# Kernel tuning notes

Hardware: AMD Instinct MI355X
Metric: run time of the kernel (lower is better)

The kernel has to match this reference:

```python
import jax, jax.numpy as jnp
import numpy as np

T, D, E = 16384, 4096, 64  # tokens, hidden dim, num experts


def setup_inputs() -> dict:
    key = jax.random.key(0)
    kx, kw = jax.random.split(key)
    x = jax.random.normal(kx, (T, D), dtype=jnp.float32)
    W = jax.random.normal(kw, (E, D), dtype=jnp.float32) * (1.0 / np.sqrt(D))
    b = jnp.zeros((E,), dtype=jnp.float32)
    return {"x": x, "W": W, "b": b}


def reference(x, W, b):
    # Linear: [T, D] @ [D, E] + [E] -> [T, E]
    logits = jnp.einsum("td,ed->te", x, W) + b
    probs = jax.nn.softmax(logits, axis=-1)
    # Top-2 selection over experts
    top2_vals, top2_idx = jax.lax.top_k(probs, 2)  # [T, 2]
    # Note: original applies softmax (not sum-renorm) to the top-2 probs
    norm2 = jax.nn.softmax(top2_vals, axis=-1)  # [T, 2]
    # Scatter back into a dense [T, E] gating distribution
    gating = jnp.zeros_like(probs)
    rows = jnp.arange(T)[:, None]
    gating = gating.at[rows, top2_idx].set(norm2)
    return gating
```

## Files before the change

### kernel.cpp

```cpp
#include <hip/hip_runtime.h>
#include <hip/hip_bf16.h>


typedef float  f32x4 __attribute__((ext_vector_type(4)));
typedef short  s16x8 __attribute__((ext_vector_type(8)));
typedef short  s16x4 __attribute__((ext_vector_type(4)));

#define T_TOK   16384
#define D_DIM   4096
#define E_EXP   64
#define KSPLIT  4
#define TAU     0.004f
#define WS_NEED (1024 * 1024 + 4 + 4 * T_TOK)

__device__ __forceinline__ unsigned short f2bf_rn(float f) {
    unsigned u = __builtin_bit_cast(unsigned, f);
    unsigned r = u + 0x7fffu + ((u >> 16) & 1u);
    return (unsigned short)(r >> 16);
}

__global__ __launch_bounds__(256)
void convw_kernel(const float* __restrict__ W, short* __restrict__ Whi, short* __restrict__ Wlo) {
    const int i = (blockIdx.x * 256 + threadIdx.x) * 4;
    f32x4 v = *(const f32x4*)(W + i);
    s16x4 h, l;
#pragma unroll
    for (int j = 0; j < 4; ++j) {
        unsigned short hb = f2bf_rn(v[j]);
        h[j] = (short)hb;
        float hf = __builtin_bit_cast(float, (unsigned)hb << 16);
        l[j] = (short)f2bf_rn(v[j] - hf);
    }
    *(s16x4*)(Whi + i) = h;
    *(s16x4*)(Wlo + i) = l;
}

__global__ __launch_bounds__(256, 4)
void gemm_logits(const float* __restrict__ x, const short* __restrict__ Whi,
                 const short* __restrict__ Wlo, float* __restrict__ out) {
    const int lane = threadIdx.x & 63;
    const int wid  = threadIdx.x >> 6;
    const int r16  = lane & 15;
    const int kb8  = (lane >> 4) << 3;
    const int trow = blockIdx.x * 64 + wid * 16 + r16;
    const int kbase = blockIdx.y * (D_DIM / KSPLIT);

    const float* ax = x   + (long)trow * D_DIM + kbase + kb8;
    const short* bh = Whi + (long)r16  * D_DIM + kbase + kb8;
    const short* bl = Wlo + (long)r16  * D_DIM + kbase + kb8;

    f32x4 acc[4];
#pragma unroll
    for (int n = 0; n < 4; ++n) acc[n] = (f32x4){0.f, 0.f, 0.f, 0.f};

    for (int ks = 0; ks < D_DIM / KSPLIT; ks += 32) {
        f32x4 a0 = *(const f32x4*)(ax + ks);
        f32x4 a1 = *(const f32x4*)(ax + ks + 4);
        s16x8 ahi, alo;
#pragma unroll
        for (int j = 0; j < 8; ++j) {
            float f = (j < 4) ? a0[j] : a1[j - 4];
            unsigned u = __builtin_bit_cast(unsigned, f);
            float hf = __builtin_bit_cast(float, u & 0xffff0000u);
            ahi[j] = (short)(u >> 16);
            alo[j] = (short)(__builtin_bit_cast(unsigned, f - hf) >> 16);
        }
#pragma unroll
        for (int n = 0; n < 4; ++n) {
            s16x8 bhi = *(const s16x8*)(bh + (long)n * 16 * D_DIM + ks);
            s16x8 blo = *(const s16x8*)(bl + (long)n * 16 * D_DIM + ks);
            acc[n] = __builtin_amdgcn_mfma_f32_16x16x32_bf16(ahi, bhi, acc[n], 0, 0, 0);
            acc[n] = __builtin_amdgcn_mfma_f32_16x16x32_bf16(alo, bhi, acc[n], 0, 0, 0);
            acc[n] = __builtin_amdgcn_mfma_f32_16x16x32_bf16(ahi, blo, acc[n], 0, 0, 0);
        }
    }

    const int orow = blockIdx.x * 64 + wid * 16 + ((lane >> 4) << 2);
#pragma unroll
    for (int n = 0; n < 4; ++n)
#pragma unroll
        for (int r = 0; r < 4; ++r)
            atomicAdd(out + (long)(orow + r) * E_EXP + n * 16 + r16, acc[n][r]);
}

__device__ __forceinline__ void argmax64(float& v, int& i) {
#pragma unroll
    for (int s = 32; s > 0; s >>= 1) {
        float ov = __shfl_xor(v, s);
        int   oi = __shfl_xor(i, s);
        if (ov > v || (ov == v && oi < i)) { v = ov; i = oi; }
    }
}

__device__ __forceinline__ float wave_gate_write(float l, int lane, float* __restrict__ outrow) {
    float v1 = l; int i1 = lane; argmax64(v1, i1);
    float v2 = (lane == i1) ? -INFINITY : l; int i2 = lane; argmax64(v2, i2);
    float v3 = (lane == i1 || lane == i2) ? -INFINITY : l; int i3 = lane; argmax64(v3, i3);
    (void)i3;

    float ex = __expf(l - v1);
    float Z = ex;
#pragma unroll
    for (int s = 32; s > 0; s >>= 1) Z += __shfl_xor(Z, s);

    float p1 = 1.0f / Z;
    float p2 = __expf(v2 - v1) / Z;
    float g1 = 1.0f / (1.0f + __expf(p2 - p1));
    float g2 = 1.0f / (1.0f + __expf(p1 - p2));

    outrow[lane] = (lane == i1) ? g1 : (lane == i2) ? g2 : 0.0f;
    return v2 - v3;
}

__global__ __launch_bounds__(256)
void finalize_router(float* __restrict__ out, const float* __restrict__ b,
                     int* __restrict__ flagc, int* __restrict__ flaglist) {
    const int lane = threadIdx.x & 63;
    const int t = blockIdx.x * 4 + (threadIdx.x >> 6);
    float l = out[(long)t * E_EXP + lane] + b[lane];
    float gap = wave_gate_write(l, lane, out + (long)t * E_EXP);
    if (gap < TAU && lane == 0) {
        int pos = atomicAdd(flagc, 1);
        flaglist[pos] = t;
    }
}

__device__ __forceinline__ void exact_row(const float* __restrict__ x, const float* __restrict__ W,
                                          const float* __restrict__ b, float* __restrict__ out,
                                          int t, int lane, int w, float (*lds)[64]) {
    const float* xr = x + (long)t * D_DIM + w * 1024;
    const float* wr = W + (long)lane * D_DIM + w * 1024;
    float acc = 0.f;
    for (int k = 0; k < 1024; k += 4) {
        f32x4 xv = *(const f32x4*)(xr + k);
        f32x4 wv = *(const f32x4*)(wr + k);
        acc += xv[0]*wv[0] + xv[1]*wv[1] + xv[2]*wv[2] + xv[3]*wv[3];
    }
    lds[w][lane] = acc;
    __syncthreads();
    if (w == 0) {
        float l = lds[0][lane] + lds[1][lane] + lds[2][lane] + lds[3][lane] + b[lane];
        wave_gate_write(l, lane, out + (long)t * E_EXP);
    }
    __syncthreads();
}

__global__ __launch_bounds__(256)
void fallback_exact(const float* __restrict__ x, const float* __restrict__ W,
                    const float* __restrict__ b, float* __restrict__ out,
                    const int* __restrict__ flags) {
    const int count = flags[0];
    const int lane = threadIdx.x & 63;
    const int w = threadIdx.x >> 6;
    __shared__ float lds[4][64];
    for (int fi = blockIdx.x; fi < count; fi += gridDim.x)
        exact_row(x, W, b, out, flags[1 + fi], lane, w, lds);
}

__global__ __launch_bounds__(256)
void exact_all(const float* __restrict__ x, const float* __restrict__ W,
               const float* __restrict__ b, float* __restrict__ out) {
    const int lane = threadIdx.x & 63;
    const int w = threadIdx.x >> 6;
    __shared__ float lds[4][64];
    for (int t = blockIdx.x; t < T_TOK; t += gridDim.x)
        exact_row(x, W, b, out, t, lane, w, lds);
}

extern "C" void kernel_launch(void* const* d_in, const int* in_sizes, int n_in,
                              void* d_out, int out_size, void* d_ws, size_t ws_size,
                              hipStream_t stream) {
    const float* x = (const float*)d_in[0];
    const float* W = (const float*)d_in[1];
    const float* b = (const float*)d_in[2];
    float* out = (float*)d_out;

    if (ws_size < (size_t)WS_NEED) {
        exact_all<<<2048, 256, 0, stream>>>(x, W, b, out);
        return;
    }

    char* ws = (char*)d_ws;
    short* Whi = (short*)ws;
    short* Wlo = (short*)(ws + 512 * 1024);
    int* flagc    = (int*)(ws + 1024 * 1024);
    int* flaglist = flagc + 1;

    hipMemsetAsync(out, 0, (size_t)T_TOK * E_EXP * sizeof(float), stream);
    hipMemsetAsync(flagc, 0, sizeof(int), stream);

    convw_kernel<<<256, 256, 0, stream>>>(W, Whi, Wlo);
    gemm_logits<<<dim3(T_TOK / 64, KSPLIT), 256, 0, stream>>>(x, Whi, Wlo, out);
    finalize_router<<<T_TOK / 4, 256, 0, stream>>>(out, b, flagc, flaglist);
    fallback_exact<<<256, 256, 0, stream>>>(x, W, b, out, flagc);
}
```

Before: 534.5 us.

## Stage split-bf16 W tiles in LDS and give each wave 64 tokens

The GEMM is restructured so each wave computes a 64-token by 64-expert tile. The W hi/lo bf16 tiles are staged into double-buffered, XOR-swizzled LDS with global_load_lds, so each W fragment is reused across four token sub-tiles instead of being re-read from global memory per 16 tokens. K-split goes from 4 to 8 and the fallback grid is enlarged. The cost is more registers, lower occupancy (launch bound 2), extra block barriers, and twice as many atomic partial-sum adds into the output.

```diff
diff --git a/kernel.cpp b/kernel.cpp
--- a/kernel.cpp
+++ b/kernel.cpp
@@ -5,11 +5,15 @@
 typedef float  f32x4 __attribute__((ext_vector_type(4)));
 typedef short  s16x8 __attribute__((ext_vector_type(8)));
 typedef short  s16x4 __attribute__((ext_vector_type(4)));
+typedef unsigned int u32;
 
 #define T_TOK   16384
 #define D_DIM   4096
 #define E_EXP   64
-#define KSPLIT  4
+#define KSPLIT  8
+#define KSLICE  (D_DIM / KSPLIT)
+#define KCHUNK  128
+#define NCHUNK  (KSLICE / KCHUNK)
 #define TAU     0.004f
 #define WS_NEED (1024 * 1024 + 4 + 4 * T_TOK)
 
@@ -17,6 +21,11 @@
     unsigned u = __builtin_bit_cast(unsigned, f);
     unsigned r = u + 0x7fffu + ((u >> 16) & 1u);
     return (unsigned short)(r >> 16);
+}
+
+__device__ __forceinline__ void gl16(const void* g, void* l) {
+    __builtin_amdgcn_global_load_lds((const __attribute__((address_space(1))) u32*)g,
+                                     (__attribute__((address_space(3))) u32*)l, 16, 0, 0);
 }
 
 __global__ __launch_bounds__(256)
@@ -35,52 +44,95 @@
     *(s16x4*)(Wlo + i) = l;
 }
 
-__global__ __launch_bounds__(256, 4)
+__global__ __launch_bounds__(256, 2)
 void gemm_logits(const float* __restrict__ x, const short* __restrict__ Whi,
                  const short* __restrict__ Wlo, float* __restrict__ out) {
+    __shared__ __align__(16) short ldsb[2][2][64 * 128];
     const int lane = threadIdx.x & 63;
     const int wid  = threadIdx.x >> 6;
     const int r16  = lane & 15;
-    const int kb8  = (lane >> 4) << 3;
-    const int trow = blockIdx.x * 64 + wid * 16 + r16;
-    const int kbase = blockIdx.y * (D_DIM / KSPLIT);
-
-    const float* ax = x   + (long)trow * D_DIM + kbase + kb8;
-    const short* bh = Whi + (long)r16  * D_DIM + kbase + kb8;
-    const short* bl = Wlo + (long)r16  * D_DIM + kbase + kb8;
-
-    f32x4 acc[4];
-#pragma unroll
-    for (int n = 0; n < 4; ++n) acc[n] = (f32x4){0.f, 0.f, 0.f, 0.f};
-
-    for (int ks = 0; ks < D_DIM / KSPLIT; ks += 32) {
-        f32x4 a0 = *(const f32x4*)(ax + ks);
-        f32x4 a1 = *(const f32x4*)(ax + ks + 4);
-        s16x8 ahi, alo;
-#pragma unroll
-        for (int j = 0; j < 8; ++j) {
-            float f = (j < 4) ? a0[j] : a1[j - 4];
-            unsigned u = __builtin_bit_cast(unsigned, f);
-            float hf = __builtin_bit_cast(float, u & 0xffff0000u);
-            ahi[j] = (short)(u >> 16);
-            alo[j] = (short)(__builtin_bit_cast(unsigned, f - hf) >> 16);
+    const int q16  = lane >> 4;
+    const int tb   = blockIdx.x * 256 + wid * 64;
+    const int kbase = blockIdx.y * KSLICE;
+
+    const float* ax[4];
+#pragma unroll
+    for (int m = 0; m < 4; ++m)
+        ax[m] = x + (long)(tb + m * 16 + r16) * D_DIM + kbase + q16 * 8;
+
+    f32x4 acc[4][4];
+#pragma unroll
+    for (int m = 0; m < 4; ++m)
+#pragma unroll
+        for (int n = 0; n < 4; ++n) acc[m][n] = (f32x4){0.f, 0.f, 0.f, 0.f};
+
+#define STAGE(c_, bb_)                                                              \
+    {                                                                               \
+        _Pragma("unroll")                                                           \
+        for (int r = 0; r < 4; ++r) {                                               \
+            const int o  = wid * 4096 + r * 1024 + lane * 16;    \
+            const int e  = o >> 8;                                                  \
+            const int cs = (o & 255) ^ ((e & 7) << 4);         \
+            const long gb = (long)e * (D_DIM * 2) + (long)(kbase + (c_)*KCHUNK) * 2 + cs; \
+            const int lb = wid * 4096 + r * 1024;                                   \
+            gl16((const char*)Whi + gb, (char*)&ldsb[bb_][0][0] + lb);              \
+            gl16((const char*)Wlo + gb, (char*)&ldsb[bb_][1][0] + lb);              \
+        }                                                                           \
+    }
+
+    STAGE(0, 0);
+    __syncthreads();
+
+#pragma unroll
+    for (int c = 0; c < NCHUNK; ++c) {
+        const int buf = c & 1;
+        if (c + 1 < NCHUNK) STAGE(c + 1, buf ^ 1);
+
+#pragma unroll
+        for (int s = 0; s < 4; ++s) {
+            const int ko = c * KCHUNK + s * 32;
+            s16x8 ahi[4], alo[4];
+#pragma unroll
+            for (int m = 0; m < 4; ++m) {
+                f32x4 a0 = *(const f32x4*)(ax[m] + ko);
+                f32x4 a1 = *(const f32x4*)(ax[m] + ko + 4);
+#pragma unroll
+                for (int j = 0; j < 8; ++j) {
+                    float f = (j < 4) ? a0[j] : a1[j - 4];
+                    u32 u = __builtin_bit_cast(u32, f);
+                    float hf = __builtin_bit_cast(float, u & 0xffff0000u);
+                    ahi[m][j] = (short)(u >> 16);
+                    alo[m][j] = (short)(__builtin_bit_cast(u32, f - hf) >> 16);
+                }
+            }
+            const int crow = s * 64 + q16 * 16;
+#pragma unroll
+            for (int n = 0; n < 4; ++n) {
+                const int e   = n * 16 + r16;
+                const int off = e * 256 + (crow ^ ((e & 7) << 4));
+                s16x8 bhi = *(const s16x8*)((const char*)&ldsb[buf][0][0] + off);
+                s16x8 blo = *(const s16x8*)((const char*)&ldsb[buf][1][0] + off);
+#pragma unroll
+                for (int m = 0; m < 4; ++m) {
+                    acc[m][n] = __builtin_amdgcn_mfma_f32_16x16x32_bf16(ahi[m], bhi, acc[m][n], 0, 0, 0);
+                    acc[m][n] = __builtin_amdgcn_mfma_f32_16x16x32_bf16(alo[m], bhi, acc[m][n], 0, 0, 0);
+                    acc[m][n] = __builtin_amdgcn_mfma_f32_16x16x32_bf16(ahi[m], blo, acc[m][n], 0, 0, 0);
+                }
+            }
         }
-#pragma unroll
-        for (int n = 0; n < 4; ++n) {
-            s16x8 bhi = *(const s16x8*)(bh + (long)n * 16 * D_DIM + ks);
-            s16x8 blo = *(const s16x8*)(bl + (long)n * 16 * D_DIM + ks);
-            acc[n] = __builtin_amdgcn_mfma_f32_16x16x32_bf16(ahi, bhi, acc[n], 0, 0, 0);
-            acc[n] = __builtin_amdgcn_mfma_f32_16x16x32_bf16(alo, bhi, acc[n], 0, 0, 0);
-            acc[n] = __builtin_amdgcn_mfma_f32_16x16x32_bf16(ahi, blo, acc[n], 0, 0, 0);
-        }
-    }
-
-    const int orow = blockIdx.x * 64 + wid * 16 + ((lane >> 4) << 2);
-#pragma unroll
-    for (int n = 0; n < 4; ++n)
-#pragma unroll
-        for (int r = 0; r < 4; ++r)
-            atomicAdd(out + (long)(orow + r) * E_EXP + n * 16 + r16, acc[n][r]);
+        __syncthreads();
+    }
+
+#pragma unroll
+    for (int m = 0; m < 4; ++m) {
+        const long rb = (long)(tb + m * 16 + q16 * 4);
+#pragma unroll
+        for (int n = 0; n < 4; ++n)
+#pragma unroll
+            for (int r = 0; r < 4; ++r)
+                atomicAdd(out + (rb + r) * E_EXP + n * 16 + r16, acc[m][n][r]);
+    }
+#undef STAGE
 }
 
 __device__ __forceinline__ void argmax64(float& v, int& i) {
@@ -190,7 +242,7 @@
     hipMemsetAsync(flagc, 0, sizeof(int), stream);
 
     convw_kernel<<<256, 256, 0, stream>>>(W, Whi, Wlo);
-    gemm_logits<<<dim3(T_TOK / 64, KSPLIT), 256, 0, stream>>>(x, Whi, Wlo, out);
+    gemm_logits<<<dim3(T_TOK / 256, KSPLIT), 256, 0, stream>>>(x, Whi, Wlo, out);
     finalize_router<<<T_TOK / 4, 256, 0, stream>>>(out, b, flagc, flaglist);
-    fallback_exact<<<256, 256, 0, stream>>>(x, W, b, out, flagc);
-}
+    fallback_exact<<<1024, 256, 0, stream>>>(x, W, b, out, flagc);
+}
```

Result: faster. 477.7 us (-10.6%).
